# Kernel tuning notes

Measured on AMD Instinct MI355X. Metric: run time of the kernel, lower is better.

## Reference

```python
import jax, jax.numpy as jnp
import numpy as np

IN_CH, OUT_CH, K, DIL, COND = 16, 16, 3, 4, 8
B, T_OUT = 32, 65536
PAD = DIL * (K - 1)


def setup_inputs() -> dict:
    key = jax.random.key(0)
    ks = jax.random.split(key, 6)
    return {
        "x": jax.random.normal(ks[0], (B, IN_CH, T_OUT + PAD), dtype=jnp.float32),
        "p": jax.random.normal(ks[1], (B, COND), dtype=jnp.float32),
        "W1": jax.random.normal(ks[2], (COND, IN_CH), dtype=jnp.float32) * 0.3,
        "b1": jax.random.normal(ks[3], (IN_CH,), dtype=jnp.float32) * 0.1,
        "W2": jax.random.normal(ks[4], (IN_CH, IN_CH * OUT_CH * K), dtype=jnp.float32) * 0.1,
        "b2": jax.random.normal(ks[5], (IN_CH * OUT_CH * K,), dtype=jnp.float32) * 0.05,
    }


def reference(x, p, W1, b1, W2, b2):
    # hypernetwork: per-sample conv weights from condition vector p
    h = p @ W1 + b1                      # [B, in_ch]
    h = jnp.where(h > 0, h, 0.2 * h)     # LeakyReLU(0.2)
    w = (h @ W2 + b2).reshape(B, IN_CH * K, OUT_CH)  # [B, in_ch*K, out_ch]

    # im2col-style gather of K dilated shifted slices, concatenated on channel dim
    start, end = PAD, x.shape[-1]
    x_cat = jnp.concatenate(
        [x[:, :, start - i * DIL : end - i * DIL] for i in range(K)], axis=1
    )  # [B, in_ch*K, T_out]

    # batched GEMM: [B, T, in_ch*K] x [B, in_ch*K, out_ch] -> output [B, out_ch, T]
    y = jnp.einsum("bct,bco->bot", x_cat, w)
    return y
```

## Files before the change

kernel.cpp:

```cpp
#include <hip/hip_runtime.h>


#define NB 32
#define IN_CH 16
#define OUT_CH 16
#define KW 3
#define DIL 4
#define COND 8
#define T_OUT 65536
#define PADT 8
#define XT (T_OUT + PADT)
#define W2COLS (IN_CH * OUT_CH * KW)
#define TPB 256
#define TPT 4
#define T_PER_BLOCK (TPB * TPT)
#define BLOCKS_PER_B (T_OUT / T_PER_BLOCK)

__global__ __launch_bounds__(TPB)
void hyperconv_kernel(const float* __restrict__ x,
                      const float* __restrict__ p,
                      const float* __restrict__ W1,
                      const float* __restrict__ b1,
                      const float* __restrict__ W2,
                      const float* __restrict__ b2,
                      float* __restrict__ y)
{
    __shared__ float h_lds[IN_CH];
    __shared__ float w_lds[W2COLS];

    const int tid    = threadIdx.x;
    const int b      = blockIdx.x / BLOCKS_PER_B;
    const int tchunk = blockIdx.x % BLOCKS_PER_B;

    if (tid < IN_CH) {
        float acc = b1[tid];
#pragma unroll
        for (int j = 0; j < COND; ++j)
            acc += p[b * COND + j] * W1[j * IN_CH + tid];
        h_lds[tid] = acc > 0.f ? acc : 0.2f * acc;
    }
    __syncthreads();

#pragma unroll
    for (int r = 0; r < 3; ++r) {
        const int n = tid * 3 + r;
        float acc = b2[n];
#pragma unroll
        for (int c = 0; c < IN_CH; ++c)
            acc += h_lds[c] * W2[c * W2COLS + n];
        w_lds[n] = acc;
    }
    __syncthreads();

    const int t0 = tchunk * T_PER_BLOCK + tid * TPT;
    const float* xb = x + (size_t)b * IN_CH * XT + t0;

    float4 acc[OUT_CH];
#pragma unroll
    for (int o = 0; o < OUT_CH; ++o) acc[o] = make_float4(0.f, 0.f, 0.f, 0.f);

#pragma unroll
    for (int c = 0; c < IN_CH; ++c) {
        const float4 a0 = *(const float4*)(xb + c * XT);
        const float4 a1 = *(const float4*)(xb + c * XT + 4);
        const float4 a2 = *(const float4*)(xb + c * XT + 8);
        const float4 vs[KW] = {a2, a1, a0};
#pragma unroll
        for (int i = 0; i < KW; ++i) {
            const float4 v = vs[i];
            const float* wrow = &w_lds[(i * IN_CH + c) * OUT_CH];
#pragma unroll
            for (int og = 0; og < 4; ++og) {
                const float4 wv = *(const float4*)(wrow + og * 4);
                float4* a = &acc[og * 4];
                a[0].x += v.x * wv.x; a[0].y += v.y * wv.x;
                a[0].z += v.z * wv.x; a[0].w += v.w * wv.x;
                a[1].x += v.x * wv.y; a[1].y += v.y * wv.y;
                a[1].z += v.z * wv.y; a[1].w += v.w * wv.y;
                a[2].x += v.x * wv.z; a[2].y += v.y * wv.z;
                a[2].z += v.z * wv.z; a[2].w += v.w * wv.z;
                a[3].x += v.x * wv.w; a[3].y += v.y * wv.w;
                a[3].z += v.z * wv.w; a[3].w += v.w * wv.w;
            }
        }
    }

    float* yb = y + (size_t)b * OUT_CH * T_OUT + t0;
#pragma unroll
    for (int o = 0; o < OUT_CH; ++o)
        *(float4*)(yb + o * T_OUT) = acc[o];
}

extern "C" void kernel_launch(void* const* d_in, const int* in_sizes, int n_in,
                              void* d_out, int out_size, void* d_ws, size_t ws_size,
                              hipStream_t stream) {
    const float* x  = (const float*)d_in[0];
    const float* p  = (const float*)d_in[1];
    const float* W1 = (const float*)d_in[2];
    const float* b1 = (const float*)d_in[3];
    const float* W2 = (const float*)d_in[4];
    const float* b2 = (const float*)d_in[5];
    float* y = (float*)d_out;

    dim3 grid(NB * BLOCKS_PER_B);
    dim3 block(TPB);
    hyperconv_kernel<<<grid, block, 0, stream>>>(x, p, W1, b1, W2, b2, y);
}
```

Before: 246.9 us.

## Split output channels across thread halves to cut accumulator registers

Each block now assigns half its threads to the first eight output channels and half to the last eight, so each thread keeps eight float4 accumulators instead of sixteen. A launch-bounds occupancy hint is added and the channel loop is only partially unrolled, both aimed at lowering register pressure and raising waves in flight to hide memory latency. In exchange each x element is loaded by two threads, which relies on cache hits, and the per-block hypernetwork weight computation runs on twice as many blocks.

```diff
diff --git a/kernel.cpp b/kernel.cpp
--- a/kernel.cpp
+++ b/kernel.cpp
@@ -5,7 +5,6 @@
 #define IN_CH 16
 #define OUT_CH 16
 #define KW 3
-#define DIL 4
 #define COND 8
 #define T_OUT 65536
 #define PADT 8
@@ -13,10 +12,12 @@
 #define W2COLS (IN_CH * OUT_CH * KW)
 #define TPB 256
 #define TPT 4
-#define T_PER_BLOCK (TPB * TPT)
+#define O_PER_THREAD 8
+#define TS_PER_BLOCK 128
+#define T_PER_BLOCK (TS_PER_BLOCK * TPT)
 #define BLOCKS_PER_B (T_OUT / T_PER_BLOCK)
 
-__global__ __launch_bounds__(TPB)
+__global__ __launch_bounds__(TPB, 8)
 void hyperconv_kernel(const float* __restrict__ x,
                       const float* __restrict__ p,
                       const float* __restrict__ W1,
@@ -28,9 +29,9 @@
     __shared__ float h_lds[IN_CH];
     __shared__ float w_lds[W2COLS];
 
-    const int tid    = threadIdx.x;
-    const int b      = blockIdx.x / BLOCKS_PER_B;
-    const int tchunk = blockIdx.x % BLOCKS_PER_B;
+    const int tid   = threadIdx.x;
+    const int b     = blockIdx.x >> 7;
+    const int chunk = blockIdx.x & (BLOCKS_PER_B - 1);
 
     if (tid < IN_CH) {
         float acc = b1[tid];
@@ -52,42 +53,51 @@
     }
     __syncthreads();
 
-    const int t0 = tchunk * T_PER_BLOCK + tid * TPT;
+    const int ohalf = tid >> 7;
+    const int ts    = tid & (TS_PER_BLOCK - 1);
+    const int t0    = chunk * T_PER_BLOCK + ts * TPT;
     const float* xb = x + (size_t)b * IN_CH * XT + t0;
+    const float* wbase = w_lds + ohalf * O_PER_THREAD;
 
-    float4 acc[OUT_CH];
+    float4 acc[O_PER_THREAD];
 #pragma unroll
-    for (int o = 0; o < OUT_CH; ++o) acc[o] = make_float4(0.f, 0.f, 0.f, 0.f);
+    for (int o = 0; o < O_PER_THREAD; ++o) acc[o] = make_float4(0.f, 0.f, 0.f, 0.f);
 
+#pragma unroll 4
+    for (int c = 0; c < IN_CH; ++c) {
+        const float* q = xb + c * XT;
+        const float4 a0 = *(const float4*)(q);
+        const float4 a1 = *(const float4*)(q + 4);
+        const float4 a2 = *(const float4*)(q + 8);
 #pragma unroll
-    for (int c = 0; c < IN_CH; ++c) {
-        const float4 a0 = *(const float4*)(xb + c * XT);
-        const float4 a1 = *(const float4*)(xb + c * XT + 4);
-        const float4 a2 = *(const float4*)(xb + c * XT + 8);
-        const float4 vs[KW] = {a2, a1, a0};
-#pragma unroll
-        for (int i = 0; i < KW; ++i) {
-            const float4 v = vs[i];
-            const float* wrow = &w_lds[(i * IN_CH + c) * OUT_CH];
-#pragma unroll
-            for (int og = 0; og < 4; ++og) {
-                const float4 wv = *(const float4*)(wrow + og * 4);
-                float4* a = &acc[og * 4];
-                a[0].x += v.x * wv.x; a[0].y += v.y * wv.x;
-                a[0].z += v.z * wv.x; a[0].w += v.w * wv.x;
-                a[1].x += v.x * wv.y; a[1].y += v.y * wv.y;
-                a[1].z += v.z * wv.y; a[1].w += v.w * wv.y;
-                a[2].x += v.x * wv.z; a[2].y += v.y * wv.z;
-                a[2].z += v.z * wv.z; a[2].w += v.w * wv.z;
-                a[3].x += v.x * wv.w; a[3].y += v.y * wv.w;
-                a[3].z += v.z * wv.w; a[3].w += v.w * wv.w;
-            }
+        for (int k = 0; k < KW; ++k) {
+            const int i = 2 - k;
+            const float4 v = (k == 0) ? a0 : (k == 1) ? a1 : a2;
+            const float* wr = wbase + (i * IN_CH + c) * OUT_CH;
+            const float4 w0 = *(const float4*)(wr);
+            const float4 w1 = *(const float4*)(wr + 4);
+            acc[0].x += v.x * w0.x; acc[0].y += v.y * w0.x;
+            acc[0].z += v.z * w0.x; acc[0].w += v.w * w0.x;
+            acc[1].x += v.x * w0.y; acc[1].y += v.y * w0.y;
+            acc[1].z += v.z * w0.y; acc[1].w += v.w * w0.y;
+            acc[2].x += v.x * w0.z; acc[2].y += v.y * w0.z;
+            acc[2].z += v.z * w0.z; acc[2].w += v.w * w0.z;
+            acc[3].x += v.x * w0.w; acc[3].y += v.y * w0.w;
+            acc[3].z += v.z * w0.w; acc[3].w += v.w * w0.w;
+            acc[4].x += v.x * w1.x; acc[4].y += v.y * w1.x;
+            acc[4].z += v.z * w1.x; acc[4].w += v.w * w1.x;
+            acc[5].x += v.x * w1.y; acc[5].y += v.y * w1.y;
+            acc[5].z += v.z * w1.y; acc[5].w += v.w * w1.y;
+            acc[6].x += v.x * w1.z; acc[6].y += v.y * w1.z;
+            acc[6].z += v.z * w1.z; acc[6].w += v.w * w1.z;
+            acc[7].x += v.x * w1.w; acc[7].y += v.y * w1.w;
+            acc[7].z += v.z * w1.w; acc[7].w += v.w * w1.w;
         }
     }
 
-    float* yb = y + (size_t)b * OUT_CH * T_OUT + t0;
+    float* yb = y + (size_t)b * OUT_CH * T_OUT + (size_t)(ohalf * O_PER_THREAD) * T_OUT + t0;
 #pragma unroll
-    for (int o = 0; o < OUT_CH; ++o)
+    for (int o = 0; o < O_PER_THREAD; ++o)
         *(float4*)(yb + o * T_OUT) = acc[o];
 }
 
```

New measurement: 371.3 us. +50.4%, slower.
